# Performance work log

Measured on AMD Instinct MI355X. Metric: run time of the kernel, lower is better.

The kernel has to match this reference:

```python
import jax, jax.numpy as jnp
import numpy as np

# dims per init_kwargs / input_specs
B, C, H, W = 8, 256, 56, 56
K = 3            # kernel_size
S = 1            # stride
D = 1            # dilation
HEAD = 1
MID = int(C * 0.2)   # se_ratio bottleneck = 51
GAIN = float(np.sqrt(2.0))  # calculate_gain('relu')


def setup_inputs() -> dict:
    key = jax.random.key(0)
    ks = jax.random.split(key, 6)
    sc = 0.05
    return {
        "x": jax.random.normal(ks[0], (B, C, H, W), jnp.float32),
        # channel branch: 1x1 convs stored as dense matrices
        "w1": jax.random.normal(ks[1], (MID, C), jnp.float32) * sc,
        "b1": jnp.zeros((MID,), jnp.float32),
        "w2": jax.random.normal(ks[2], (C * K * K, MID), jnp.float32) * sc,
        "b2": jnp.zeros((C * K * K,), jnp.float32),
        # spatial branch: 1x1 conv c -> head*k^2
        "ws": jax.random.normal(ks[3], (HEAD * K * K, C), jnp.float32) * sc,
        "bs": jnp.zeros((HEAD * K * K,), jnp.float32),
        # FilterNorm running_std parameter (channel branch): randn * gain/k
        "fn_std": jax.random.normal(ks[4], (C * K * K,), jnp.float32) * (GAIN / K),
    }


def _ddf_mul(x, cf, sf):
    """Decoupled dynamic filter, 'mul' combine.
    x: (B,C,H,W), cf: (B,C,K,K) channel filter, sf: (B,K*K,Ho,Wo) spatial filter.
    out[b,c,i,j] = sum_{u,v} x[b,c, i*S+(u-(K-1)/2)*D, j*S+(v-(K-1)/2)*D] * cf[b,c,u,v] * sf[b,u*K+v,i,j]
    Accumulate over the K*K taps to avoid materializing the unfolded tensor."""
    p = D * (K - 1) // 2
    xp = jnp.pad(x, ((0, 0), (0, 0), (p, p), (p, p)))
    Ho, Wo = H // S, W // S
    out = jnp.zeros((B, C, Ho, Wo), x.dtype)
    for u in range(K):
        for v in range(K):
            patch = xp[:, :, u * D:u * D + S * Ho:S, v * D:v * D + S * Wo:S]
            out = out + patch * cf[:, :, u, v][:, :, None, None] * sf[:, u * K + v][:, None]
    return out


def reference(x, w1, b1, w2, b2, ws, bs, fn_std):
    # ---- channel branch: SE-style filter generation ----
    pooled = x.mean((2, 3))                                  # (B,C) global avg pool
    y = jax.nn.relu(pooled @ w1.T + b1)                      # (B,MID)
    y = (y @ w2.T + b2).reshape(B, C, K * K)                 # (B,C,K^2)
    # FilterNorm 'channel': normalize over K^2 (torch std -> ddof=1), learned std
    y = (y - y.mean(-1, keepdims=True)) / (y.std(-1, ddof=1, keepdims=True) + 1e-10)
    cf = (y.reshape(B, C * K * K) * fn_std).reshape(B, C, K, K)
    # ---- spatial branch: 1x1 conv (stride S) + FilterNorm 'spatial' ----
    xs = x[:, :, ::S, ::S]
    sf = jnp.einsum('bchw,nc->bnhw', xs, ws) + bs[None, :, None, None]  # (B,K^2,Ho,Wo)
    sf = sf.reshape(B, HEAD, K * K, H // S, W // S)
    sf = (sf - sf.mean(2, keepdims=True)) / (sf.std(2, ddof=1, keepdims=True) + 1e-10)
    sf = sf.reshape(B, HEAD * K * K, H // S, W // S) * (GAIN / K)
    # ---- fused per-pixel gather-multiply-reduce (head=1 -> no group reshape) ----
    return _ddf_mul(x, cf, sf)
```

## Files before the change

kernel.cpp:

```cpp
#include <hip/hip_runtime.h>
#include <math.h>

#define BB   8
#define CC   256
#define HH   56
#define WW   56
#define KK   3
#define MIDN 51
#define NTAP (KK*KK)
#define CKK  (CC*NTAP)
#define HW   (HH*WW)
#define SPIX 64
#define NSTR (HW/SPIX)
#define CPR  128
#define XSTR 65
#define NCPB 4
#define TILE 3364

__global__ __launch_bounds__(256) void k_sf(const float* __restrict__ x,
                                            const float* __restrict__ ws,
                                            const float* __restrict__ bs,
                                            float* __restrict__ sf,
                                            float* __restrict__ poolpart) {
    int blk = blockIdx.x;
    int s = blk % NSTR;
    int b = blk / NSTR;
    int t = threadIdx.x;
    int p = t & 63;
    int q = t >> 6;
    __shared__ float xs[CPR * XSTR];
    __shared__ float wss[NTAP][CC];
    __shared__ float accq[NTAP * 4 * SPIX];
    for (int idx = t; idx < NTAP * CC; idx += 256)
        ((float*)wss)[idx] = ws[idx];
    float acc[NTAP];
    #pragma unroll
    for (int n = 0; n < NTAP; ++n) acc[n] = 0.f;
    const float* xb = x + ((size_t)b * CC) * HW + s * SPIX;
    #pragma unroll
    for (int r = 0; r < 2; ++r) {
        if (r) __syncthreads();
        float vv[32];
        #pragma unroll
        for (int c = 0; c < 32; ++c)
            vv[c] = xb[(size_t)(r * CPR + q * 32 + c) * HW + p];
        #pragma unroll
        for (int c = 0; c < 32; ++c)
            xs[(q * 32 + c) * XSTR + p] = vv[c];
        __syncthreads();
        if (t < CPR) {
            float sum = 0.f;
            #pragma unroll 8
            for (int pp = 0; pp < SPIX; ++pp) sum += xs[t * XSTR + pp];
            poolpart[((size_t)(b * NSTR + s)) * CC + r * CPR + t] = sum;
        }
        #pragma unroll 4
        for (int c = 0; c < 32; ++c) {
            float xv = xs[(q * 32 + c) * XSTR + p];
            #pragma unroll
            for (int n = 0; n < NTAP; ++n)
                acc[n] += xv * wss[n][r * CPR + q * 32 + c];
        }
    }
    #pragma unroll
    for (int n = 0; n < NTAP; ++n) accq[(n * 4 + q) * SPIX + p] = acc[n];
    __syncthreads();
    if (t < SPIX) {
        float y[NTAP];
        #pragma unroll
        for (int n = 0; n < NTAP; ++n) {
            float v = bs[n];
            #pragma unroll
            for (int qq = 0; qq < 4; ++qq) v += accq[(n * 4 + qq) * SPIX + t];
            y[n] = v;
        }
        float mean = 0.f;
        #pragma unroll
        for (int n = 0; n < NTAP; ++n) mean += y[n];
        mean *= (1.f / NTAP);
        float var = 0.f;
        #pragma unroll
        for (int n = 0; n < NTAP; ++n) { float d = y[n] - mean; var += d * d; }
        float inv = 0.47140452079103173f /
                    (sqrtf(var * (1.f / (NTAP - 1))) + 1e-10f);
        #pragma unroll
        for (int n = 0; n < NTAP; ++n)
            sf[((size_t)(b * NTAP + n)) * HW + s * SPIX + t] = (y[n] - mean) * inv;
    }
}

__global__ __launch_bounds__(512) void k_ddf(const float* __restrict__ x,
                                             const float* __restrict__ poolpart,
                                             const float* __restrict__ w1,
                                             const float* __restrict__ b1,
                                             const float* __restrict__ w2,
                                             const float* __restrict__ b2,
                                             const float* __restrict__ fn_std,
                                             const float* __restrict__ sf,
                                             float* __restrict__ out) {
    int blk = blockIdx.x;
    int b = blk / (CC / NCPB), cg = blk % (CC / NCPB);
    int c0 = cg * NCPB;
    int t = threadIdx.x;
    __shared__ float xt[NCPB][TILE];
    __shared__ float ps[CC];
    __shared__ float y1s[64];
    __shared__ float y2s[NCPB * NTAP];
    __shared__ float cfs[NCPB * NTAP];
    for (int idx = t; idx < NCPB * TILE; idx += 512) ((float*)xt)[idx] = 0.f;
    __syncthreads();
    const float4* xp4 = (const float4*)(x + ((size_t)(b * CC + c0)) * HW);
    for (int i4 = t; i4 < NCPB * HW / 4; i4 += 512) {
        float4 v = xp4[i4];
        int k = i4 / (HW / 4);
        int rem4 = i4 - k * (HW / 4);
        int r = rem4 / (WW / 4);
        int col = 4 * (rem4 - r * (WW / 4));
        float* d = &xt[k][(r + 1) * 58 + col + 1];
        d[0] = v.x; d[1] = v.y; d[2] = v.z; d[3] = v.w;
    }
    if (t < CC) {
        float s = 0.f;
        const float* pp = poolpart + ((size_t)b * NSTR) * CC + t;
        for (int st = 0; st < NSTR; ++st) s += pp[(size_t)st * CC];
        ps[t] = s * (1.0f / HW);
    }
    __syncthreads();
    if (t < MIDN) {
        float a = b1[t];
        const float* wr = w1 + t * CC;
        for (int c2 = 0; c2 < CC; ++c2) a += ps[c2] * wr[c2];
        y1s[t] = fmaxf(a, 0.f);
    }
    __syncthreads();
    if (t < NCPB * NTAP) {
        int row = c0 * NTAP + t;
        float a = b2[row];
        const float* r = w2 + (size_t)row * MIDN;
        #pragma unroll 3
        for (int m = 0; m < MIDN; ++m) a += y1s[m] * r[m];
        y2s[t] = a;
    }
    __syncthreads();
    if (t < NCPB) {
        float y2[NTAP];
        #pragma unroll
        for (int q = 0; q < NTAP; ++q) y2[q] = y2s[t * NTAP + q];
        float mean = 0.f;
        #pragma unroll
        for (int q = 0; q < NTAP; ++q) mean += y2[q];
        mean *= (1.f / NTAP);
        float var = 0.f;
        #pragma unroll
        for (int q = 0; q < NTAP; ++q) { float d = y2[q] - mean; var += d * d; }
        float inv = 1.f / (sqrtf(var * (1.f / (NTAP - 1))) + 1e-10f);
        #pragma unroll
        for (int q = 0; q < NTAP; ++q)
            cfs[t * NTAP + q] = (y2[q] - mean) * inv * fn_std[(c0 + t) * NTAP + q];
    }
    __syncthreads();
    float cf9[NCPB][NTAP];
    #pragma unroll
    for (int k = 0; k < NCPB; ++k)
        #pragma unroll
        for (int n = 0; n < NTAP; ++n) cf9[k][n] = cfs[k * NTAP + n];
    const float* sfb = sf + (size_t)b * NTAP * HW;
    float* op = out + ((size_t)(b * CC + c0)) * HW;
    for (int idx = t; idx < HW; idx += 512) {
        int i = idx / WW, j = idx - i * WW;
        float s9[NTAP];
        #pragma unroll
        for (int n = 0; n < NTAP; ++n) s9[n] = sfb[(size_t)n * HW + idx];
        float acc[NCPB];
        #pragma unroll
        for (int k = 0; k < NCPB; ++k) acc[k] = 0.f;
        #pragma unroll
        for (int u = 0; u < KK; ++u)
            #pragma unroll
            for (int v = 0; v < KK; ++v) {
                int n = u * KK + v;
                int o = (i + u) * 58 + (j + v);
                #pragma unroll
                for (int k = 0; k < NCPB; ++k)
                    acc[k] += xt[k][o] * (cf9[k][n] * s9[n]);
            }
        #pragma unroll
        for (int k = 0; k < NCPB; ++k) op[(size_t)k * HW + idx] = acc[k];
    }
}

extern "C" void kernel_launch(void* const* d_in, const int* in_sizes, int n_in,
                              void* d_out, int out_size, void* d_ws, size_t ws_size,
                              hipStream_t stream) {
    const float* x      = (const float*)d_in[0];
    const float* w1     = (const float*)d_in[1];
    const float* b1     = (const float*)d_in[2];
    const float* w2     = (const float*)d_in[3];
    const float* b2     = (const float*)d_in[4];
    const float* ws     = (const float*)d_in[5];
    const float* bs     = (const float*)d_in[6];
    const float* fn_std = (const float*)d_in[7];
    float* out = (float*)d_out;

    float* wsf      = (float*)d_ws;
    float* sf       = wsf;
    float* poolpart = sf + 225792;

    k_sf<<<BB * NSTR, 256, 0, stream>>>(x, ws, bs, sf, poolpart);
    k_ddf<<<BB * (CC / NCPB), 512, 0, stream>>>(x, poolpart, w1, b1, w2, b2,
                                                fn_std, sf, out);
}
```

Baseline: 114.9 us.

## Vectorize DDF main loop: 4 pixels per thread with float4 padded shared tiles

```diff
diff --git a/kernel.cpp b/kernel.cpp
--- a/kernel.cpp
+++ b/kernel.cpp
@@ -15,7 +15,8 @@
 #define CPR  128
 #define XSTR 65
 #define NCPB 4
-#define TILE 3364
+#define TROW 68
+#define TPL  (58*TROW)
 
 __global__ __launch_bounds__(256) void k_sf(const float* __restrict__ x,
                                             const float* __restrict__ ws,
@@ -89,25 +90,29 @@
     }
 }
 
-__global__ __launch_bounds__(512) void k_ddf(const float* __restrict__ x,
-                                             const float* __restrict__ poolpart,
-                                             const float* __restrict__ w1,
-                                             const float* __restrict__ b1,
-                                             const float* __restrict__ w2,
-                                             const float* __restrict__ b2,
-                                             const float* __restrict__ fn_std,
-                                             const float* __restrict__ sf,
-                                             float* __restrict__ out) {
+__global__ __launch_bounds__(512, 4) void k_ddf(const float* __restrict__ x,
+                                                const float* __restrict__ poolpart,
+                                                const float* __restrict__ w1,
+                                                const float* __restrict__ b1,
+                                                const float* __restrict__ w2,
+                                                const float* __restrict__ b2,
+                                                const float* __restrict__ fn_std,
+                                                const float* __restrict__ sf,
+                                                float* __restrict__ out) {
     int blk = blockIdx.x;
     int b = blk / (CC / NCPB), cg = blk % (CC / NCPB);
     int c0 = cg * NCPB;
     int t = threadIdx.x;
-    __shared__ float xt[NCPB][TILE];
+    __shared__ __align__(16) float xt[NCPB][TPL];
     __shared__ float ps[CC];
     __shared__ float y1s[64];
     __shared__ float y2s[NCPB * NTAP];
     __shared__ float cfs[NCPB * NTAP];
-    for (int idx = t; idx < NCPB * TILE; idx += 512) ((float*)xt)[idx] = 0.f;
+    {
+        float4 z4 = make_float4(0.f, 0.f, 0.f, 0.f);
+        float4* xt4 = (float4*)xt;
+        for (int i4 = t; i4 < NCPB * TPL / 4; i4 += 512) xt4[i4] = z4;
+    }
     __syncthreads();
     const float4* xp4 = (const float4*)(x + ((size_t)(b * CC + c0)) * HW);
     for (int i4 = t; i4 < NCPB * HW / 4; i4 += 512) {
@@ -116,8 +121,7 @@
         int rem4 = i4 - k * (HW / 4);
         int r = rem4 / (WW / 4);
         int col = 4 * (rem4 - r * (WW / 4));
-        float* d = &xt[k][(r + 1) * 58 + col + 1];
-        d[0] = v.x; d[1] = v.y; d[2] = v.z; d[3] = v.w;
+        *(float4*)&xt[k][(r + 1) * TROW + col + 4] = v;
     }
     if (t < CC) {
         float s = 0.f;
@@ -166,26 +170,41 @@
         for (int n = 0; n < NTAP; ++n) cf9[k][n] = cfs[k * NTAP + n];
     const float* sfb = sf + (size_t)b * NTAP * HW;
     float* op = out + ((size_t)(b * CC + c0)) * HW;
-    for (int idx = t; idx < HW; idx += 512) {
-        int i = idx / WW, j = idx - i * WW;
-        float s9[NTAP];
-        #pragma unroll
-        for (int n = 0; n < NTAP; ++n) s9[n] = sfb[(size_t)n * HW + idx];
-        float acc[NCPB];
-        #pragma unroll
-        for (int k = 0; k < NCPB; ++k) acc[k] = 0.f;
-        #pragma unroll
-        for (int u = 0; u < KK; ++u)
+    for (int g4 = t; g4 < HW / 4; g4 += 512) {
+        int i = g4 / (WW / 4);
+        int j0 = 4 * (g4 - i * (WW / 4));
+        int pix = i * WW + j0;
+        float acc[NCPB][4];
+        #pragma unroll
+        for (int k = 0; k < NCPB; ++k) {
+            acc[k][0] = 0.f; acc[k][1] = 0.f; acc[k][2] = 0.f; acc[k][3] = 0.f;
+        }
+        #pragma unroll
+        for (int u = 0; u < KK; ++u) {
+            float4 s0 = *(const float4*)&sfb[(size_t)(u * 3 + 0) * HW + pix];
+            float4 s1 = *(const float4*)&sfb[(size_t)(u * 3 + 1) * HW + pix];
+            float4 s2 = *(const float4*)&sfb[(size_t)(u * 3 + 2) * HW + pix];
+            int base = (i + u) * TROW + j0;
             #pragma unroll
-            for (int v = 0; v < KK; ++v) {
-                int n = u * KK + v;
-                int o = (i + u) * 58 + (j + v);
-                #pragma unroll
-                for (int k = 0; k < NCPB; ++k)
-                    acc[k] += xt[k][o] * (cf9[k][n] * s9[n]);
+            for (int k = 0; k < NCPB; ++k) {
+                float4 A = *(const float4*)&xt[k][base];
+                float4 B = *(const float4*)&xt[k][base + 4];
+                float4 C = *(const float4*)&xt[k][base + 8];
+                float w0 = A.w, w1 = B.x, w2 = B.y, w3 = B.z, w4 = B.w, w5 = C.x;
+                float c_0 = cf9[k][u * 3 + 0];
+                float c_1 = cf9[k][u * 3 + 1];
+                float c_2 = cf9[k][u * 3 + 2];
+                acc[k][0] += w0 * (c_0 * s0.x) + w1 * (c_1 * s1.x) + w2 * (c_2 * s2.x);
+                acc[k][1] += w1 * (c_0 * s0.y) + w2 * (c_1 * s1.y) + w3 * (c_2 * s2.y);
+                acc[k][2] += w2 * (c_0 * s0.z) + w3 * (c_1 * s1.z) + w4 * (c_2 * s2.z);
+                acc[k][3] += w3 * (c_0 * s0.w) + w4 * (c_1 * s1.w) + w5 * (c_2 * s2.w);
             }
-        #pragma unroll
-        for (int k = 0; k < NCPB; ++k) op[(size_t)k * HW + idx] = acc[k];
+        }
+        #pragma unroll
+        for (int k = 0; k < NCPB; ++k) {
+            float4 o4 = make_float4(acc[k][0], acc[k][1], acc[k][2], acc[k][3]);
+            *(float4*)&op[(size_t)k * HW + pix] = o4;
+        }
     }
 }
 
```

Result: slower. 142.3 us (+23.8%).

## Use sliding register window over rows in DDF kernel with 448-thread blocks

Applied to the files above, without the earlier changes.

```diff
diff --git a/kernel.cpp b/kernel.cpp
--- a/kernel.cpp
+++ b/kernel.cpp
@@ -89,15 +89,15 @@
     }
 }
 
-__global__ __launch_bounds__(512) void k_ddf(const float* __restrict__ x,
-                                             const float* __restrict__ poolpart,
-                                             const float* __restrict__ w1,
-                                             const float* __restrict__ b1,
-                                             const float* __restrict__ w2,
-                                             const float* __restrict__ b2,
-                                             const float* __restrict__ fn_std,
-                                             const float* __restrict__ sf,
-                                             float* __restrict__ out) {
+__global__ __launch_bounds__(448, 3) void k_ddf(const float* __restrict__ x,
+                                                const float* __restrict__ poolpart,
+                                                const float* __restrict__ w1,
+                                                const float* __restrict__ b1,
+                                                const float* __restrict__ w2,
+                                                const float* __restrict__ b2,
+                                                const float* __restrict__ fn_std,
+                                                const float* __restrict__ sf,
+                                                float* __restrict__ out) {
     int blk = blockIdx.x;
     int b = blk / (CC / NCPB), cg = blk % (CC / NCPB);
     int c0 = cg * NCPB;
@@ -107,10 +107,10 @@
     __shared__ float y1s[64];
     __shared__ float y2s[NCPB * NTAP];
     __shared__ float cfs[NCPB * NTAP];
-    for (int idx = t; idx < NCPB * TILE; idx += 512) ((float*)xt)[idx] = 0.f;
+    for (int idx = t; idx < NCPB * TILE; idx += 448) ((float*)xt)[idx] = 0.f;
     __syncthreads();
     const float4* xp4 = (const float4*)(x + ((size_t)(b * CC + c0)) * HW);
-    for (int i4 = t; i4 < NCPB * HW / 4; i4 += 512) {
+    for (int i4 = t; i4 < NCPB * HW / 4; i4 += 448) {
         float4 v = xp4[i4];
         int k = i4 / (HW / 4);
         int rem4 = i4 - k * (HW / 4);
@@ -164,28 +164,48 @@
     for (int k = 0; k < NCPB; ++k)
         #pragma unroll
         for (int n = 0; n < NTAP; ++n) cf9[k][n] = cfs[k * NTAP + n];
-    const float* sfb = sf + (size_t)b * NTAP * HW;
-    float* op = out + ((size_t)(b * CC + c0)) * HW;
-    for (int idx = t; idx < HW; idx += 512) {
-        int i = idx / WW, j = idx - i * WW;
+    int j = t % WW;
+    int oct = t / WW;
+    int i0 = oct * 7;
+    const float* sfb = sf + (size_t)b * NTAP * HW + j;
+    float* op = out + ((size_t)(b * CC + c0)) * HW + j;
+    float wr0[NCPB][3], wr1[NCPB][3], wr2[NCPB][3];
+    #pragma unroll
+    for (int k = 0; k < NCPB; ++k)
+        #pragma unroll
+        for (int c = 0; c < 3; ++c) {
+            wr0[k][c] = xt[k][(i0    ) * 58 + j + c];
+            wr1[k][c] = xt[k][(i0 + 1) * 58 + j + c];
+        }
+    #pragma unroll
+    for (int s = 0; s < 7; ++s) {
+        int i = i0 + s;
+        #pragma unroll
+        for (int k = 0; k < NCPB; ++k)
+            #pragma unroll
+            for (int c = 0; c < 3; ++c)
+                wr2[k][c] = xt[k][(i + 2) * 58 + j + c];
         float s9[NTAP];
         #pragma unroll
-        for (int n = 0; n < NTAP; ++n) s9[n] = sfb[(size_t)n * HW + idx];
-        float acc[NCPB];
-        #pragma unroll
-        for (int k = 0; k < NCPB; ++k) acc[k] = 0.f;
-        #pragma unroll
-        for (int u = 0; u < KK; ++u)
-            #pragma unroll
-            for (int v = 0; v < KK; ++v) {
-                int n = u * KK + v;
-                int o = (i + u) * 58 + (j + v);
-                #pragma unroll
-                for (int k = 0; k < NCPB; ++k)
-                    acc[k] += xt[k][o] * (cf9[k][n] * s9[n]);
+        for (int n = 0; n < NTAP; ++n) s9[n] = sfb[(size_t)n * HW + i * WW];
+        #pragma unroll
+        for (int k = 0; k < NCPB; ++k) {
+            float a = 0.f;
+            #pragma unroll
+            for (int c = 0; c < 3; ++c) {
+                a += wr0[k][c] * (cf9[k][0 * 3 + c] * s9[0 * 3 + c]);
+                a += wr1[k][c] * (cf9[k][1 * 3 + c] * s9[1 * 3 + c]);
+                a += wr2[k][c] * (cf9[k][2 * 3 + c] * s9[2 * 3 + c]);
             }
-        #pragma unroll
-        for (int k = 0; k < NCPB; ++k) op[(size_t)k * HW + idx] = acc[k];
+            op[(size_t)k * HW + i * WW] = a;
+        }
+        #pragma unroll
+        for (int k = 0; k < NCPB; ++k)
+            #pragma unroll
+            for (int c = 0; c < 3; ++c) {
+                wr0[k][c] = wr1[k][c];
+                wr1[k][c] = wr2[k][c];
+            }
     }
 }
 
@@ -207,6 +227,6 @@
     float* poolpart = sf + 225792;
 
     k_sf<<<BB * NSTR, 256, 0, stream>>>(x, ws, bs, sf, poolpart);
-    k_ddf<<<BB * (CC / NCPB), 512, 0, stream>>>(x, poolpart, w1, b1, w2, b2,
+    k_ddf<<<BB * (CC / NCPB), 448, 0, stream>>>(x, poolpart, w1, b1, w2, b2,
                                                 fn_std, sf, out);
 }
```

Measured after the change: 113.8 us, median of 2. About the same (-1.0%).
